# Kernel tuning notes

Measured on AMD Instinct MI355X. Metric: run time of the kernel, lower is better.

## Reference

```python
import jax, jax.numpy as jnp
import numpy as np

MAX_SEQ_LEN = 1024
EMBED_DIM = 64


def setup_inputs() -> dict:
    key = jax.random.key(0)
    k1, k2, k3 = jax.random.split(key, 3)
    B, H, L, D = 2, 16, 1024, EMBED_DIM
    q = jax.random.normal(k1, (B, H, L, D), dtype=jnp.float32)
    k = jax.random.normal(k2, (B, H, L, D), dtype=jnp.float32)
    pos_emb = jax.random.normal(k3, (2 * MAX_SEQ_LEN - 1, D), dtype=jnp.float32)
    return {"q": q, "k": k, "pos_emb": pos_emb}


def reference(q, k, pos_emb):
    q_len = q.shape[2]
    k_len = k.shape[2]
    # relative distance index matrix, shifted and clamped into table range
    idx = jnp.arange(q_len)[:, None] - jnp.arange(k_len)[None, :] + (MAX_SEQ_LEN - 1)
    idx = jnp.clip(idx, 0, 2 * MAX_SEQ_LEN - 2)
    rel_emb = pos_emb[idx]  # [q_len, k_len, D]  (the O(Q*K*D) gather)
    # per-query batched contraction over head dim D
    bias = jnp.einsum('bhqd,qkd->bhqk', q, rel_emb)
    return bias / jnp.sqrt(jnp.asarray(EMBED_DIM, dtype=q.dtype))
```

## Files before the change

kernel.cpp:

```cpp
#include <hip/hip_runtime.h>
#include <hip/hip_bf16.h>
#include <stdint.h>


#define LSEQ 1024
#define DDIM 64

typedef __attribute__((ext_vector_type(8))) short bf16x8;
typedef __attribute__((ext_vector_type(16))) float f32x16;

__device__ __forceinline__ unsigned short f2b(float f) {
  union { float f; unsigned u; } c; c.f = f;
  unsigned u = c.u;
  u += 0x7fffu + ((u >> 16) & 1u);
  return (unsigned short)(u >> 16);
}

__global__ __launch_bounds__(256) void cvt_kernel(
    const float4* __restrict__ q4, const float4* __restrict__ p4,
    ushort4* __restrict__ qb, ushort4* __restrict__ pb) {
  int i = blockIdx.x * 256 + threadIdx.x;
  if (i < 524288) {
    float4 v = q4[i];
    ushort4 o;
    o.x = f2b(v.x * 0.125f); o.y = f2b(v.y * 0.125f);
    o.z = f2b(v.z * 0.125f); o.w = f2b(v.w * 0.125f);
    qb[i] = o;
  } else {
    int j = i - 524288;
    if (j < 32752) {
      float4 v = p4[j];
      ushort4 o;
      o.x = f2b(v.x); o.y = f2b(v.y); o.z = f2b(v.z); o.w = f2b(v.w);
      pb[j] = o;
    }
  }
}

__global__ __launch_bounds__(256) void rpe_kernel(
    const short* __restrict__ Qb, const short* __restrict__ Pb,
    float* __restrict__ out) {
  __shared__ short lds[4][2][2048];
  const int q    = blockIdx.x;
  const int tid  = (int)threadIdx.x;
  const int lane = tid & 63;
  const int wave = tid >> 6;
  const int l31  = lane & 31;
  const int hi   = lane >> 5;
  const int nbase = wave << 8;

  const int lane_off = ((lane >> 3) << 7) + ((((lane & 7) ^ (lane >> 3))) << 4);
  const char* Pc = (const char*)Pb;

  {
    const int lo = q + 992 - nbase;
    const char* src = Pc + ((size_t)lo << 7) + lane_off;
#pragma unroll
    for (int j = 0; j < 4; ++j)
      __builtin_amdgcn_global_load_lds(
          (const __attribute__((address_space(1))) void*)(src + (j << 10)),
          (__attribute__((address_space(3))) void*)&lds[wave][0][j << 9],
          16, 0, 0);
  }

  bf16x8 a[4];
  const short* qp = Qb + ((l31 << 10) + q) * DDIM + (hi << 3);
#pragma unroll
  for (int s = 0; s < 4; ++s)
    a[s] = *(const bf16x8*)(qp + 16 * s);

  const int rr = 31 - l31;
  const int rx = rr & 7;

#pragma unroll
  for (int t = 0; t < 8; ++t) {
    {
      const int tn = (t + 1) & 7;
      const int b  = (t + 1) & 1;
      const int lo = q + 992 - nbase - (tn << 5);
      const char* src = Pc + ((size_t)lo << 7) + lane_off;
#pragma unroll
      for (int j = 0; j < 4; ++j)
        __builtin_amdgcn_global_load_lds(
            (const __attribute__((address_space(1))) void*)(src + (j << 10)),
            (__attribute__((address_space(3))) void*)&lds[wave][b][j << 9],
            16, 0, 0);
    }
    if (t == 0) asm volatile("s_waitcnt vmcnt(4)" ::: "memory");
    else        asm volatile("s_waitcnt vmcnt(20)" ::: "memory");

    const short* base = &lds[wave][t & 1][rr << 6];
    f32x16 acc;
#pragma unroll
    for (int r = 0; r < 16; ++r) acc[r] = 0.0f;
#pragma unroll
    for (int s = 0; s < 4; ++s) {
      bf16x8 bfr = *(const bf16x8*)(base + (((hi + 2 * s) ^ rx) << 3));
      acc = __builtin_amdgcn_mfma_f32_32x32x16_bf16(a[s], bfr, acc, 0, 0, 0);
    }
    float* obase = out + ((size_t)hi << 22) + (q << 10) + nbase + (t << 5) + l31;
#pragma unroll
    for (int r = 0; r < 16; ++r) {
      const int m = (r & 3) + 8 * (r >> 2);
      obase[(size_t)m << 20] = acc[r];
    }
  }
}

extern "C" void kernel_launch(void* const* d_in, const int* in_sizes, int n_in,
                              void* d_out, int out_size, void* d_ws, size_t ws_size,
                              hipStream_t stream) {
  const float* qin = (const float*)d_in[0];
  const float* pin = (const float*)d_in[2];

  short* qb = (short*)d_ws;
  short* pb = (short*)d_ws + 2097152;

  cvt_kernel<<<2176, 256, 0, stream>>>((const float4*)qin, (const float4*)pin,
                                       (ushort4*)qb, (ushort4*)pb);
  rpe_kernel<<<1024, 256, 0, stream>>>(qb, pb, (float*)d_out);
}
```

Baseline: 38.44 us.

## Deepen LDS prefetch to two stages, pair output stores, remap block order

The P-tile prefetch now runs two stages ahead: two tiles are staged before the loop, and the next load is issued after each compute step. The redundant wrap-around load on the last iteration is gone, and the vmcnt waits are retuned to match. Results from two consecutive tiles are held in separate accumulators and written together, so each pair of stores is issued as one batch. The block-to-query mapping is interleaved, which changes how concurrent blocks spread their pos_emb reads and output writes. All of this aims to overlap global loads with MFMA work and stores, at the cost of more registers and hand-counted waits that depend on the exact order of memory operations.

```diff
diff --git a/kernel.cpp b/kernel.cpp
--- a/kernel.cpp
+++ b/kernel.cpp
@@ -41,7 +41,8 @@
     const short* __restrict__ Qb, const short* __restrict__ Pb,
     float* __restrict__ out) {
   __shared__ short lds[4][2][2048];
-  const int q    = blockIdx.x;
+  const int bid  = (int)blockIdx.x;
+  const int q    = ((bid & 7) << 7) + (bid >> 3);
   const int tid  = (int)threadIdx.x;
   const int lane = tid & 63;
   const int wave = tid >> 6;
@@ -52,16 +53,18 @@
   const int lane_off = ((lane >> 3) << 7) + ((((lane & 7) ^ (lane >> 3))) << 4);
   const char* Pc = (const char*)Pb;
 
-  {
-    const int lo = q + 992 - nbase;
+  auto STAGE = [&](int tt, int buf) {
+    const int lo = q + 992 - nbase - (tt << 5);
     const char* src = Pc + ((size_t)lo << 7) + lane_off;
 #pragma unroll
     for (int j = 0; j < 4; ++j)
       __builtin_amdgcn_global_load_lds(
           (const __attribute__((address_space(1))) void*)(src + (j << 10)),
-          (__attribute__((address_space(3))) void*)&lds[wave][0][j << 9],
+          (__attribute__((address_space(3))) void*)&lds[wave][buf][j << 9],
           16, 0, 0);
-  }
+  };
+
+  STAGE(0, 0);
 
   bf16x8 a[4];
   const short* qp = Qb + ((l31 << 10) + q) * DDIM + (hi << 3);
@@ -69,41 +72,43 @@
   for (int s = 0; s < 4; ++s)
     a[s] = *(const bf16x8*)(qp + 16 * s);
 
+  STAGE(1, 1);
+
   const int rr = 31 - l31;
   const int rx = rr & 7;
 
+  f32x16 accA, accB;
 #pragma unroll
   for (int t = 0; t < 8; ++t) {
-    {
-      const int tn = (t + 1) & 7;
-      const int b  = (t + 1) & 1;
-      const int lo = q + 992 - nbase - (tn << 5);
-      const char* src = Pc + ((size_t)lo << 7) + lane_off;
+    if (t == 0 || t == 1 || t == 3 || t == 5)
+      asm volatile("s_waitcnt vmcnt(4)" ::: "memory");
+    else if (t == 7)
+      asm volatile("s_waitcnt vmcnt(0)" ::: "memory");
+    else
+      asm volatile("s_waitcnt vmcnt(36)" ::: "memory");
+
+    f32x16& acc = (t & 1) ? accB : accA;
 #pragma unroll
-      for (int j = 0; j < 4; ++j)
-        __builtin_amdgcn_global_load_lds(
-            (const __attribute__((address_space(1))) void*)(src + (j << 10)),
-            (__attribute__((address_space(3))) void*)&lds[wave][b][j << 9],
-            16, 0, 0);
-    }
-    if (t == 0) asm volatile("s_waitcnt vmcnt(4)" ::: "memory");
-    else        asm volatile("s_waitcnt vmcnt(20)" ::: "memory");
+    for (int r = 0; r < 16; ++r) acc[r] = 0.0f;
 
     const short* base = &lds[wave][t & 1][rr << 6];
-    f32x16 acc;
-#pragma unroll
-    for (int r = 0; r < 16; ++r) acc[r] = 0.0f;
 #pragma unroll
     for (int s = 0; s < 4; ++s) {
       bf16x8 bfr = *(const bf16x8*)(base + (((hi + 2 * s) ^ rx) << 3));
       acc = __builtin_amdgcn_mfma_f32_32x32x16_bf16(a[s], bfr, acc, 0, 0, 0);
     }
-    float* obase = out + ((size_t)hi << 22) + (q << 10) + nbase + (t << 5) + l31;
+
+    if (t & 1) {
+      float* ob = out + ((size_t)hi << 22) + (q << 10) + nbase + ((t - 1) << 5) + l31;
 #pragma unroll
-    for (int r = 0; r < 16; ++r) {
-      const int m = (r & 3) + 8 * (r >> 2);
-      obase[(size_t)m << 20] = acc[r];
+      for (int r = 0; r < 16; ++r) {
+        const int m = (r & 3) + 8 * (r >> 2);
+        ob[(size_t)m << 20]      = accA[r];
+        ob[((size_t)m << 20) + 32] = accB[r];
+      }
     }
+
+    if (t < 6) STAGE(t + 2, t & 1);
   }
 }
 
```

After: 33.86 us. -11.9%, faster.
